# Kernel tuning notes

Measured on AMD Instinct MI355X. Metric: run time of the kernel, lower is better.

## Reference

```python
import jax, jax.numpy as jnp
import numpy as np

N, C, H, W = 16, 64, 128, 128
KH, KW = 3, 3
SH, SW = 1, 1


def _window_flat_indices(H, W):
    """Flat input indices of each element of each sliding window.
    Returns int32 array [num_windows, KH*KW]."""
    Ho = (H - KH) // SH + 1
    Wo = (W - KW) // SW + 1
    i = np.arange(Ho) * SH
    j = np.arange(Wo) * SW
    a = np.arange(KH)
    b = np.arange(KW)
    rows = i[:, None, None, None] + a[None, None, :, None]   # [Ho,1,KH,1]
    cols = j[None, :, None, None] + b[None, None, None, :]   # [1,Wo,1,KW]
    flat = (rows * W + cols).reshape(Ho * Wo, KH * KW)       # [Wn, K]
    return jnp.asarray(flat, dtype=jnp.int32)


def setup_inputs() -> dict:
    key = jax.random.key(0)
    x = jax.random.normal(key, (N, C, H, W), dtype=jnp.float32)
    return {"x": x}


def reference(x):
    n, c, h, w = x.shape
    flat = _window_flat_indices(h, w)            # [Wn, K]
    Wn, K = flat.shape
    nc = n * c
    xf = x.reshape(nc, h * w)                    # [NC, HW]
    patches = xf[:, flat]                        # [NC, Wn, K]
    amax = jnp.argmax(patches, axis=-1)          # [NC, Wn] local winner
    amin = jnp.argmin(patches, axis=-1)          # [NC, Wn]
    warp = jnp.arange(Wn)[None, :]
    win_max = flat[warp, amax]                   # [NC, Wn] flat input idx of max winner
    win_min = flat[warp, amin]                   # [NC, Wn]
    idx = jnp.concatenate([win_max, win_min], axis=1)                      # [NC, 2Wn]
    vals = jnp.concatenate([jnp.ones((Wn,), x.dtype), -jnp.ones((Wn,), x.dtype)])
    counts = jnp.zeros((nc, h * w), x.dtype)
    counts = counts.at[jnp.arange(nc)[:, None], idx].add(vals[None, :])
    return counts.reshape(n, c, h, w)
```

## Files before the change

kernel.cpp:

```cpp
#include <hip/hip_runtime.h>


#define HH 128
#define WW 128
#define HO 126
#define WO 126
#define PLANE (HH * WW)
#define HROWS 64
#define HPLANE (HROWS * WW)
#define NPLANES (16 * 64)
#define BLOCK 512

__device__ __forceinline__ void scan9(float w0, float w1, float w2,
                                      float w3, float w4, float w5,
                                      float w6, float w7, float w8,
                                      int base, int bias, int* __restrict__ cnt) {
    float vmax = w0, vmin = w0;
    int omax = 0, omin = 0;
#define STEP(v, off)                                      \
    do {                                                  \
        if ((v) > vmax) { vmax = (v); omax = (off); }     \
        if ((v) < vmin) { vmin = (v); omin = (off); }     \
    } while (0)
    STEP(w1, 1);
    STEP(w2, 2);
    STEP(w3, WW);
    STEP(w4, WW + 1);
    STEP(w5, WW + 2);
    STEP(w6, 2 * WW);
    STEP(w7, 2 * WW + 1);
    STEP(w8, 2 * WW + 2);
#undef STEP
    const int iM = base + omax - bias;
    if ((unsigned)iM < HPLANE) atomicAdd(&cnt[iM], 1);
    const int im = base + omin - bias;
    if ((unsigned)im < HPLANE) atomicAdd(&cnt[im], -1);
}

__global__ __launch_bounds__(BLOCK, 8)
void energy_pool2d_kernel(const float* __restrict__ x, float* __restrict__ out) {
    __shared__ int cnt[HPLANE];

    const int tid = threadIdx.x;
    const int plane = blockIdx.x >> 1;
    const int half = blockIdx.x & 1;
    const float* __restrict__ xp = x + (size_t)plane * PLANE;

    int4* c4 = (int4*)cnt;
#pragma unroll
    for (int i = 0; i < HPLANE / 4 / BLOCK; ++i)
        c4[tid + i * BLOCK] = make_int4(0, 0, 0, 0);
    __syncthreads();

    const int row0 = half ? 62 : 0;
    const int bias = half * HPLANE;

#pragma unroll
    for (int it = 0; it < 2; ++it) {
        const int t = tid + it * BLOCK;
        const int rt = t >> 5;
        const int ct = t & 31;
        const int wr0 = row0 + rt * 2;
        const int j0 = ct * 4;
        const float* __restrict__ p = xp + wr0 * WW + j0;

        const float4 a0 = *(const float4*)(p);
        const float4 a1 = *(const float4*)(p + WW);
        const float4 a2 = *(const float4*)(p + 2 * WW);
        const float4 a3 = *(const float4*)(p + 3 * WW);
        float4 b0, b1, b2, b3;
        if (ct < 31) {
            b0 = *(const float4*)(p + 4);
            b1 = *(const float4*)(p + WW + 4);
            b2 = *(const float4*)(p + 2 * WW + 4);
            b3 = *(const float4*)(p + 3 * WW + 4);
        } else {
            b0 = b1 = b2 = b3 = make_float4(0.f, 0.f, 0.f, 0.f);
        }
        const float r0[8] = {a0.x, a0.y, a0.z, a0.w, b0.x, b0.y, b0.z, b0.w};
        const float r1[8] = {a1.x, a1.y, a1.z, a1.w, b1.x, b1.y, b1.z, b1.w};
        const float r2[8] = {a2.x, a2.y, a2.z, a2.w, b2.x, b2.y, b2.z, b2.w};
        const float r3[8] = {a3.x, a3.y, a3.z, a3.w, b3.x, b3.y, b3.z, b3.w};

        const int nw = (ct < 31) ? 4 : 2;
        const int base0 = wr0 * WW + j0;
#pragma unroll
        for (int c = 0; c < 4; ++c) {
            if (c < nw) {
                scan9(r0[c], r0[c + 1], r0[c + 2],
                      r1[c], r1[c + 1], r1[c + 2],
                      r2[c], r2[c + 1], r2[c + 2], base0 + c, bias, cnt);
                scan9(r1[c], r1[c + 1], r1[c + 2],
                      r2[c], r2[c + 1], r2[c + 2],
                      r3[c], r3[c + 1], r3[c + 2], base0 + WW + c, bias, cnt);
            }
        }
    }
    __syncthreads();

    float4* __restrict__ o4 = (float4*)(out + (size_t)plane * PLANE + bias);
#pragma unroll
    for (int i = 0; i < HPLANE / 4 / BLOCK; ++i) {
        const int4 ci = c4[tid + i * BLOCK];
        o4[tid + i * BLOCK] =
            make_float4((float)ci.x, (float)ci.y, (float)ci.z, (float)ci.w);
    }
}

extern "C" void kernel_launch(void* const* d_in, const int* in_sizes, int n_in,
                              void* d_out, int out_size, void* d_ws, size_t ws_size,
                              hipStream_t stream) {
    const float* x = (const float*)d_in[0];
    float* out = (float*)d_out;
    energy_pool2d_kernel<<<NPLANES * 2, BLOCK, 0, stream>>>(x, out);
}
```

Baseline: 32.31 us.

## Process both plane halves per block with double-buffered shared counters

Each block now handles a whole plane instead of half, using two 32KB shared counter buffers. The first half's counts are written out while the second half is computed, overlapping stores with loads and atomics. Grid size halves and shared memory per block doubles to 64KB, which lowers the number of resident blocks per CU (launch bounds go from 8 to 4).

```diff
diff --git a/kernel.cpp b/kernel.cpp
--- a/kernel.cpp
+++ b/kernel.cpp
@@ -3,11 +3,8 @@
 
 #define HH 128
 #define WW 128
-#define HO 126
-#define WO 126
 #define PLANE (HH * WW)
-#define HROWS 64
-#define HPLANE (HROWS * WW)
+#define HPLANE (64 * WW)
 #define NPLANES (16 * 64)
 #define BLOCK 512
 
@@ -37,24 +34,9 @@
     if ((unsigned)im < HPLANE) atomicAdd(&cnt[im], -1);
 }
 
-__global__ __launch_bounds__(BLOCK, 8)
-void energy_pool2d_kernel(const float* __restrict__ x, float* __restrict__ out) {
-    __shared__ int cnt[HPLANE];
-
-    const int tid = threadIdx.x;
-    const int plane = blockIdx.x >> 1;
-    const int half = blockIdx.x & 1;
-    const float* __restrict__ xp = x + (size_t)plane * PLANE;
-
-    int4* c4 = (int4*)cnt;
-#pragma unroll
-    for (int i = 0; i < HPLANE / 4 / BLOCK; ++i)
-        c4[tid + i * BLOCK] = make_int4(0, 0, 0, 0);
-    __syncthreads();
-
-    const int row0 = half ? 62 : 0;
-    const int bias = half * HPLANE;
-
+__device__ __forceinline__ void compute_half(const float* __restrict__ xp,
+                                             int row0, int bias, int tid,
+                                             int* __restrict__ cnt) {
 #pragma unroll
     for (int it = 0; it < 2; ++it) {
         const int t = tid + it * BLOCK;
@@ -96,14 +78,48 @@
             }
         }
     }
+}
+
+__global__ __launch_bounds__(BLOCK, 4)
+void energy_pool2d_kernel(const float* __restrict__ x, float* __restrict__ out) {
+    __shared__ int cnt[2][HPLANE];
+
+    const int tid = threadIdx.x;
+    const int plane = blockIdx.x;
+    const float* __restrict__ xp = x + (size_t)plane * PLANE;
+    float* __restrict__ op = out + (size_t)plane * PLANE;
+
+    int4* cz = (int4*)&cnt[0][0];
+#pragma unroll
+    for (int i = 0; i < 2 * HPLANE / 4 / BLOCK; ++i)
+        cz[tid + i * BLOCK] = make_int4(0, 0, 0, 0);
     __syncthreads();
 
-    float4* __restrict__ o4 = (float4*)(out + (size_t)plane * PLANE + bias);
+    compute_half(xp, 0, 0, tid, &cnt[0][0]);
+    __syncthreads();
+
+    {
+        const int4* c4 = (const int4*)&cnt[0][0];
+        float4* __restrict__ o4 = (float4*)op;
 #pragma unroll
-    for (int i = 0; i < HPLANE / 4 / BLOCK; ++i) {
-        const int4 ci = c4[tid + i * BLOCK];
-        o4[tid + i * BLOCK] =
-            make_float4((float)ci.x, (float)ci.y, (float)ci.z, (float)ci.w);
+        for (int i = 0; i < HPLANE / 4 / BLOCK; ++i) {
+            const int4 ci = c4[tid + i * BLOCK];
+            o4[tid + i * BLOCK] =
+                make_float4((float)ci.x, (float)ci.y, (float)ci.z, (float)ci.w);
+        }
+    }
+    compute_half(xp, 62, HPLANE, tid, &cnt[1][0]);
+    __syncthreads();
+
+    {
+        const int4* c4 = (const int4*)&cnt[1][0];
+        float4* __restrict__ o4 = (float4*)(op + HPLANE);
+#pragma unroll
+        for (int i = 0; i < HPLANE / 4 / BLOCK; ++i) {
+            const int4 ci = c4[tid + i * BLOCK];
+            o4[tid + i * BLOCK] =
+                make_float4((float)ci.x, (float)ci.y, (float)ci.z, (float)ci.w);
+        }
     }
 }
 
@@ -112,5 +128,5 @@
                               hipStream_t stream) {
     const float* x = (const float*)d_in[0];
     float* out = (float*)d_out;
-    energy_pool2d_kernel<<<NPLANES * 2, BLOCK, 0, stream>>>(x, out);
+    energy_pool2d_kernel<<<NPLANES, BLOCK, 0, stream>>>(x, out);
 }
```

New measurement: 37.89 us. 1.17x slower.

## Split each half-plane into two quarter passes with double-buffered LDS and nontemporal stores

Applied to the files above, without the earlier changes.

Each block now handles its half-plane as two sequential 32-row strips, each with its own LDS counter buffer, so the writeback of one strip can overlap the atomics of the next. Barriers are replaced with an explicit lgkmcnt wait plus s_barrier, and output stores become nontemporal. This adds halo rows that are loaded twice and an extra barrier phase per strip, and the strip loop is no longer fully unrolled.

```diff
diff --git a/kernel.cpp b/kernel.cpp
--- a/kernel.cpp
+++ b/kernel.cpp
@@ -1,15 +1,14 @@
 #include <hip/hip_runtime.h>
 
 
-#define HH 128
 #define WW 128
-#define HO 126
-#define WO 126
-#define PLANE (HH * WW)
-#define HROWS 64
-#define HPLANE (HROWS * WW)
+#define PLANE (128 * 128)
+#define SROWS 32
+#define SPLANE (SROWS * WW)
 #define NPLANES (16 * 64)
 #define BLOCK 512
+
+typedef float vf4 __attribute__((ext_vector_type(4)));
 
 __device__ __forceinline__ void scan9(float w0, float w1, float w2,
                                       float w3, float w4, float w5,
@@ -32,78 +31,90 @@
     STEP(w8, 2 * WW + 2);
 #undef STEP
     const int iM = base + omax - bias;
-    if ((unsigned)iM < HPLANE) atomicAdd(&cnt[iM], 1);
+    if ((unsigned)iM < SPLANE) atomicAdd(&cnt[iM], 1);
     const int im = base + omin - bias;
-    if ((unsigned)im < HPLANE) atomicAdd(&cnt[im], -1);
+    if ((unsigned)im < SPLANE) atomicAdd(&cnt[im], -1);
 }
 
 __global__ __launch_bounds__(BLOCK, 8)
 void energy_pool2d_kernel(const float* __restrict__ x, float* __restrict__ out) {
-    __shared__ int cnt[HPLANE];
+    __shared__ int cnt[2][SPLANE];
 
     const int tid = threadIdx.x;
     const int plane = blockIdx.x >> 1;
-    const int half = blockIdx.x & 1;
+    const int hp = blockIdx.x & 1;
     const float* __restrict__ xp = x + (size_t)plane * PLANE;
-
-    int4* c4 = (int4*)cnt;
-#pragma unroll
-    for (int i = 0; i < HPLANE / 4 / BLOCK; ++i)
-        c4[tid + i * BLOCK] = make_int4(0, 0, 0, 0);
-    __syncthreads();
-
-    const int row0 = half ? 62 : 0;
-    const int bias = half * HPLANE;
+    float* __restrict__ op = out + (size_t)plane * PLANE;
 
 #pragma unroll
-    for (int it = 0; it < 2; ++it) {
-        const int t = tid + it * BLOCK;
-        const int rt = t >> 5;
-        const int ct = t & 31;
-        const int wr0 = row0 + rt * 2;
-        const int j0 = ct * 4;
-        const float* __restrict__ p = xp + wr0 * WW + j0;
+    for (int s = 0; s < 2; ++s) {
+        const int q = hp * 2 + s;
+        const int R0 = q * SROWS;
+        const int bias = R0 * WW;
+        int* __restrict__ c = &cnt[s][0];
 
-        const float4 a0 = *(const float4*)(p);
-        const float4 a1 = *(const float4*)(p + WW);
-        const float4 a2 = *(const float4*)(p + 2 * WW);
-        const float4 a3 = *(const float4*)(p + 3 * WW);
-        float4 b0, b1, b2, b3;
-        if (ct < 31) {
-            b0 = *(const float4*)(p + 4);
-            b1 = *(const float4*)(p + WW + 4);
-            b2 = *(const float4*)(p + 2 * WW + 4);
-            b3 = *(const float4*)(p + 3 * WW + 4);
-        } else {
-            b0 = b1 = b2 = b3 = make_float4(0.f, 0.f, 0.f, 0.f);
-        }
-        const float r0[8] = {a0.x, a0.y, a0.z, a0.w, b0.x, b0.y, b0.z, b0.w};
-        const float r1[8] = {a1.x, a1.y, a1.z, a1.w, b1.x, b1.y, b1.z, b1.w};
-        const float r2[8] = {a2.x, a2.y, a2.z, a2.w, b2.x, b2.y, b2.z, b2.w};
-        const float r3[8] = {a3.x, a3.y, a3.z, a3.w, b3.x, b3.y, b3.z, b3.w};
+        int4* cz = (int4*)c;
+        cz[tid] = make_int4(0, 0, 0, 0);
+        cz[tid + BLOCK] = make_int4(0, 0, 0, 0);
+        asm volatile("s_waitcnt lgkmcnt(0)" ::: "memory");
+        __builtin_amdgcn_s_barrier();
 
-        const int nw = (ct < 31) ? 4 : 2;
-        const int base0 = wr0 * WW + j0;
+        const int wrb = (q == 0) ? 0 : (R0 - 2);
+        const int wre = (q == 3) ? 126 : (R0 + SROWS);
+        const int ntiles = ((wre - wrb) >> 1) * 32;
+
+        for (int t = tid; t < ntiles; t += BLOCK) {
+            const int rt = t >> 5;
+            const int ct = t & 31;
+            const int wr0 = wrb + rt * 2;
+            const int j0 = ct * 4;
+            const float* __restrict__ p = xp + wr0 * WW + j0;
+
+            const float4 a0 = *(const float4*)(p);
+            const float4 a1 = *(const float4*)(p + WW);
+            const float4 a2 = *(const float4*)(p + 2 * WW);
+            const float4 a3 = *(const float4*)(p + 3 * WW);
+            float4 b0, b1, b2, b3;
+            if (ct < 31) {
+                b0 = *(const float4*)(p + 4);
+                b1 = *(const float4*)(p + WW + 4);
+                b2 = *(const float4*)(p + 2 * WW + 4);
+                b3 = *(const float4*)(p + 3 * WW + 4);
+            } else {
+                b0 = b1 = b2 = b3 = make_float4(0.f, 0.f, 0.f, 0.f);
+            }
+            const float r0[8] = {a0.x, a0.y, a0.z, a0.w, b0.x, b0.y, b0.z, b0.w};
+            const float r1[8] = {a1.x, a1.y, a1.z, a1.w, b1.x, b1.y, b1.z, b1.w};
+            const float r2[8] = {a2.x, a2.y, a2.z, a2.w, b2.x, b2.y, b2.z, b2.w};
+            const float r3[8] = {a3.x, a3.y, a3.z, a3.w, b3.x, b3.y, b3.z, b3.w};
+
+            const int nw = (ct < 31) ? 4 : 2;
+            const int base0 = wr0 * WW + j0;
 #pragma unroll
-        for (int c = 0; c < 4; ++c) {
-            if (c < nw) {
-                scan9(r0[c], r0[c + 1], r0[c + 2],
-                      r1[c], r1[c + 1], r1[c + 2],
-                      r2[c], r2[c + 1], r2[c + 2], base0 + c, bias, cnt);
-                scan9(r1[c], r1[c + 1], r1[c + 2],
-                      r2[c], r2[c + 1], r2[c + 2],
-                      r3[c], r3[c + 1], r3[c + 2], base0 + WW + c, bias, cnt);
+            for (int cc = 0; cc < 4; ++cc) {
+                if (cc < nw) {
+                    scan9(r0[cc], r0[cc + 1], r0[cc + 2],
+                          r1[cc], r1[cc + 1], r1[cc + 2],
+                          r2[cc], r2[cc + 1], r2[cc + 2], base0 + cc, bias, c);
+                    scan9(r1[cc], r1[cc + 1], r1[cc + 2],
+                          r2[cc], r2[cc + 1], r2[cc + 2],
+                          r3[cc], r3[cc + 1], r3[cc + 2], base0 + WW + cc, bias, c);
+                }
             }
         }
-    }
-    __syncthreads();
+        asm volatile("s_waitcnt lgkmcnt(0)" ::: "memory");
+        __builtin_amdgcn_s_barrier();
 
-    float4* __restrict__ o4 = (float4*)(out + (size_t)plane * PLANE + bias);
+        const int4* cr = (const int4*)c;
+        vf4* __restrict__ o4 = (vf4*)(op + bias);
 #pragma unroll
-    for (int i = 0; i < HPLANE / 4 / BLOCK; ++i) {
-        const int4 ci = c4[tid + i * BLOCK];
-        o4[tid + i * BLOCK] =
-            make_float4((float)ci.x, (float)ci.y, (float)ci.z, (float)ci.w);
+        for (int i = 0; i < 2; ++i) {
+            const int4 ci = cr[tid + i * BLOCK];
+            vf4 f;
+            f.x = (float)ci.x; f.y = (float)ci.y;
+            f.z = (float)ci.z; f.w = (float)ci.w;
+            __builtin_nontemporal_store(f, o4 + tid + i * BLOCK);
+        }
     }
 }
 
```

Measured after the change: 33.88 us. 4.9% more time.
